# Optimization experiments

Measured on AMD Instinct MI355X. Metric: run time of the kernel, lower is better.

The kernel has to match this reference:

```python
import jax, jax.numpy as jnp
import numpy as np

B = 131072
D = 64
NUM_REL = 32


def setup_inputs() -> dict:
    key = jax.random.key(0)
    k1, k2, k3, k4 = jax.random.split(key, 4)
    embeds1 = jax.random.normal(k1, (B, D), dtype=jnp.float32)
    embeds2 = jax.random.normal(k2, (B, D), dtype=jnp.float32)
    rels = jax.random.randint(k3, (B,), 0, NUM_REL, dtype=jnp.int32)
    # learned relation table: one D*D matrix per relation type
    rel_embeds = jax.random.normal(k4, (NUM_REL, D * D), dtype=jnp.float32)
    return {"embeds1": embeds1, "embeds2": embeds2, "rels": rels,
            "rel_embeds": rel_embeds}


def reference(embeds1, embeds2, rels, rel_embeds):
    # gather per-sample relation matrices: [B, D, D]
    rel_mats = rel_embeds[rels].reshape(-1, D, D)
    # per-sample bilinear form: score_b = e1_b^T R_b e2_b  -> [B]
    e1R = jnp.einsum("bd,bde->be", embeds1, rel_mats)
    return (e1R * embeds2).sum(axis=1)
```

## Files before the change

kernel.cpp:

```cpp
#include <hip/hip_runtime.h>
#include <hip/hip_bf16.h>
#include <cstddef>

#define BB 131072
#define DD 64
#define NREL 32
#define PADN 131584
#define NWAVE (PADN / 16)

#define BLOCKS_AC 512
#define SPB (BB / BLOCKS_AC)
#define CHUNKS 8
#define BPC (BLOCKS_AC / CHUNKS)

typedef __attribute__((ext_vector_type(8))) __bf16 bf16x8;
typedef __attribute__((ext_vector_type(4))) float f32x4;

__global__ __launch_bounds__(256) void phaseR_pre(
    const float* __restrict__ relE, __bf16* __restrict__ Rpre) {
  const int r = blockIdx.x;
  const int t = threadIdx.x;
  const float* __restrict__ R = relE + (size_t)r * (DD * DD);
  __bf16* __restrict__ dst = Rpre + (size_t)r * 8192;
#pragma unroll
  for (int i = 0; i < 16; ++i) {
    const int idx = i * 256 + t;
    const int g = idx >> 9;
    const int lane = (idx >> 3) & 63;
    const int j = idx & 7;
    const int k = (g >> 2) * 32 + (lane >> 4) * 8 + j;
    const int n = (g & 3) * 16 + (lane & 15);
    const float x = R[k * DD + n];
    const __bf16 hb = (__bf16)x;
    dst[idx] = hb;
    dst[4096 + idx] = (__bf16)(x - (float)hb);
  }
}

__global__ __launch_bounds__(256) void phaseA_hist(
    const int* __restrict__ rels, int* __restrict__ blockCnt) {
  __shared__ int hist[NREL];
  const int t = threadIdx.x;
  if (t < NREL) hist[t] = 0;
  __syncthreads();
  atomicAdd(&hist[rels[blockIdx.x * 256 + t]], 1);
  __syncthreads();
  if (t < NREL) blockCnt[blockIdx.x * NREL + t] = hist[t];
}

__global__ __launch_bounds__(256) void phaseB_scan(
    const int* __restrict__ blockCnt, int* __restrict__ blockOff,
    int* __restrict__ binBase, int* __restrict__ permPacked) {
  __shared__ int partial[CHUNKS][NREL];
  __shared__ int chunkBase[CHUNKS][NREL];
  __shared__ int binB[NREL];
  __shared__ int totS[NREL];
  __shared__ int totalPad;
  const int t = threadIdx.x;
  const int c = t >> 5;
  const int r = t & 31;
  const int b0 = c * BPC;
  int run = 0;
#pragma unroll 4
  for (int b = 0; b < BPC; ++b) run += blockCnt[(b0 + b) * NREL + r];
  partial[c][r] = run;
  __syncthreads();
  if (t < NREL) {
    int acc = 0;
#pragma unroll
    for (int i = 0; i < CHUNKS; ++i) { chunkBase[i][t] = acc; acc += partial[i][t]; }
    totS[t] = acc;
  }
  __syncthreads();
  if (t == 0) {
    int acc = 0;
#pragma unroll
    for (int i = 0; i < NREL; ++i) {
      binB[i] = acc;
      acc += (totS[i] + 15) & ~15;
    }
    totalPad = acc;
  }
  __syncthreads();
  if (t < NREL) {
    binBase[t] = binB[t];
    const int start = binB[t] + totS[t];
    const int end = binB[t] + ((totS[t] + 15) & ~15);
    for (int p = start; p < end; ++p) permPacked[p] = -1;
  }
  for (int p = totalPad + t; p < PADN; p += 256) permPacked[p] = -1;
  int run2 = chunkBase[c][r];
#pragma unroll 4
  for (int b = 0; b < BPC; ++b) {
    blockOff[(b0 + b) * NREL + r] = run2;
    run2 += blockCnt[(b0 + b) * NREL + r];
  }
}

__global__ __launch_bounds__(256) void phaseC_scatter(
    const int* __restrict__ rels, const int* __restrict__ blockOff,
    const int* __restrict__ binBase, int* __restrict__ permPacked) {
  __shared__ int cnt[NREL];
  __shared__ int baseArr[NREL];
  const int t = threadIdx.x;
  if (t < NREL) {
    cnt[t] = 0;
    baseArr[t] = binBase[t] + blockOff[blockIdx.x * NREL + t];
  }
  __syncthreads();
  const int s = blockIdx.x * SPB + t;
  const int rv = rels[s];
  const int rank = atomicAdd(&cnt[rv], 1);
  permPacked[baseArr[rv] + rank] = (rv << 17) | s;
}

__global__ __launch_bounds__(64, 4) void bilinear_mfma16(
    const float* __restrict__ e1g, const float* __restrict__ e2g,
    const __bf16* __restrict__ Rpre, const int* __restrict__ permPacked,
    float* __restrict__ out) {
  __shared__ float sA[16 * 65];
  const int lane = threadIdx.x;
  const int l15 = lane & 15;
  const int h2 = lane >> 4;
  const int pk = permPacked[blockIdx.x * 16 + l15];
  const unsigned long long vm = __ballot(pk >= 0);
  if (vm == 0ull) return;
  const int r0 = __builtin_amdgcn_readlane(pk, (int)__builtin_ctzll(vm)) >> 17;

#pragma unroll
  for (int i = 0; i < 16; ++i) {
    const int s = __builtin_amdgcn_readlane(pk, i) & 0x1FFFF;
    sA[i * 65 + lane] = e1g[(size_t)s * DD + lane];
  }
  __syncthreads();

  const bf16x8* __restrict__ bp = (const bf16x8*)(Rpre + (size_t)r0 * 8192);

  f32x4 acc[4];
#pragma unroll
  for (int nt = 0; nt < 4; ++nt)
#pragma unroll
    for (int i = 0; i < 4; ++i) acc[nt][i] = 0.f;

#pragma unroll
  for (int kc = 0; kc < 2; ++kc) {
    bf16x8 aH, aL;
    const float* p = &sA[l15 * 65 + kc * 32 + h2 * 8];
#pragma unroll
    for (int j = 0; j < 8; ++j) {
      const float x = p[j];
      const __bf16 hb = (__bf16)x;
      aH[j] = hb;
      aL[j] = (__bf16)(x - (float)hb);
    }
#pragma unroll
    for (int nt = 0; nt < 4; ++nt) {
      const int g = kc * 4 + nt;
      const bf16x8 bH = bp[g * 64 + lane];
      const bf16x8 bL = bp[512 + g * 64 + lane];
      acc[nt] = __builtin_amdgcn_mfma_f32_16x16x32_bf16(aH, bH, acc[nt], 0, 0, 0);
      acc[nt] = __builtin_amdgcn_mfma_f32_16x16x32_bf16(aH, bL, acc[nt], 0, 0, 0);
      acc[nt] = __builtin_amdgcn_mfma_f32_16x16x32_bf16(aL, bH, acc[nt], 0, 0, 0);
    }
  }

  float rp[4] = {0.f, 0.f, 0.f, 0.f};
#pragma unroll
  for (int reg = 0; reg < 4; ++reg) {
    const int si = __shfl(pk, h2 * 4 + reg) & 0x1FFFF;
    const float* er = e2g + (size_t)si * DD + l15;
#pragma unroll
    for (int nt = 0; nt < 4; ++nt)
      rp[reg] = fmaf(acc[nt][reg], er[nt * 16], rp[reg]);
  }
#pragma unroll
  for (int m = 1; m < 16; m <<= 1)
#pragma unroll
    for (int reg = 0; reg < 4; ++reg) rp[reg] += __shfl_xor(rp[reg], m);
#pragma unroll
  for (int reg = 0; reg < 4; ++reg) {
    const int pkw = __shfl(pk, h2 * 4 + reg);
    if (l15 == reg && pkw >= 0) out[pkw & 0x1FFFF] = rp[reg];
  }
}

extern "C" void kernel_launch(void* const* d_in, const int* in_sizes, int n_in,
                              void* d_out, int out_size, void* d_ws, size_t ws_size,
                              hipStream_t stream) {
  const float* e1 = (const float*)d_in[0];
  const float* e2 = (const float*)d_in[1];
  const int* rels = (const int*)d_in[2];
  const float* relE = (const float*)d_in[3];
  float* out = (float*)d_out;

  int* permPacked = (int*)d_ws;
  int* blockCnt = permPacked + PADN;
  int* blockOff = blockCnt + BLOCKS_AC * NREL;
  int* binBase = blockOff + BLOCKS_AC * NREL;
  __bf16* Rpre = (__bf16*)((char*)d_ws + (1 << 20));

  phaseR_pre<<<NREL, 256, 0, stream>>>(relE, Rpre);
  phaseA_hist<<<BLOCKS_AC, 256, 0, stream>>>(rels, blockCnt);
  phaseB_scan<<<1, 256, 0, stream>>>(blockCnt, blockOff, binBase, permPacked);
  phaseC_scatter<<<BLOCKS_AC, 256, 0, stream>>>(rels, blockOff, binBase, permPacked);
  bilinear_mfma16<<<NWAVE, 64, 0, stream>>>(e1, e2, Rpre, permPacked, out);
}
```

Baseline: 118.3 us.

## Fuse relation preprocessing into histogram kernel and pack four waves per block

The relation-matrix bf16 split is folded into the histogram kernel, which removes one kernel launch. The bilinear kernel now runs four 16-sample waves per 256-thread block and drops the LDS staging of e1 rows. Each lane loads its e1 row directly as float4 vectors and prefetches its e2 values before the MFMA loop. This cuts launch overhead, LDS traffic and the barrier, and lets the e2 loads overlap the matrix work, at the cost of less coalesced direct global loads of e1 and higher register pressure.

```diff
diff --git a/kernel.cpp b/kernel.cpp
--- a/kernel.cpp
+++ b/kernel.cpp
@@ -6,7 +6,7 @@
 #define DD 64
 #define NREL 32
 #define PADN 131584
-#define NWAVE (PADN / 16)
+#define NBLK (PADN / 64)
 
 #define BLOCKS_AC 512
 #define SPB (BB / BLOCKS_AC)
@@ -16,29 +16,9 @@
 typedef __attribute__((ext_vector_type(8))) __bf16 bf16x8;
 typedef __attribute__((ext_vector_type(4))) float f32x4;
 
-__global__ __launch_bounds__(256) void phaseR_pre(
+__global__ __launch_bounds__(256) void phaseA_hist(
+    const int* __restrict__ rels, int* __restrict__ blockCnt,
     const float* __restrict__ relE, __bf16* __restrict__ Rpre) {
-  const int r = blockIdx.x;
-  const int t = threadIdx.x;
-  const float* __restrict__ R = relE + (size_t)r * (DD * DD);
-  __bf16* __restrict__ dst = Rpre + (size_t)r * 8192;
-#pragma unroll
-  for (int i = 0; i < 16; ++i) {
-    const int idx = i * 256 + t;
-    const int g = idx >> 9;
-    const int lane = (idx >> 3) & 63;
-    const int j = idx & 7;
-    const int k = (g >> 2) * 32 + (lane >> 4) * 8 + j;
-    const int n = (g & 3) * 16 + (lane & 15);
-    const float x = R[k * DD + n];
-    const __bf16 hb = (__bf16)x;
-    dst[idx] = hb;
-    dst[4096 + idx] = (__bf16)(x - (float)hb);
-  }
-}
-
-__global__ __launch_bounds__(256) void phaseA_hist(
-    const int* __restrict__ rels, int* __restrict__ blockCnt) {
   __shared__ int hist[NREL];
   const int t = threadIdx.x;
   if (t < NREL) hist[t] = 0;
@@ -46,6 +26,25 @@
   atomicAdd(&hist[rels[blockIdx.x * 256 + t]], 1);
   __syncthreads();
   if (t < NREL) blockCnt[blockIdx.x * NREL + t] = hist[t];
+
+  if (blockIdx.x < NREL) {
+    const int r = blockIdx.x;
+    const float* __restrict__ R = relE + (size_t)r * (DD * DD);
+    __bf16* __restrict__ dst = Rpre + (size_t)r * 8192;
+#pragma unroll
+    for (int i = 0; i < 16; ++i) {
+      const int idx = i * 256 + t;
+      const int g = idx >> 9;
+      const int lane = (idx >> 3) & 63;
+      const int j = idx & 7;
+      const int k = (g >> 2) * 32 + (lane >> 4) * 8 + j;
+      const int n = (g & 3) * 16 + (lane & 15);
+      const float x = R[k * DD + n];
+      const __bf16 hb = (__bf16)x;
+      dst[idx] = hb;
+      dst[4096 + idx] = (__bf16)(x - (float)hb);
+    }
+  }
 }
 
 __global__ __launch_bounds__(256) void phaseB_scan(
@@ -114,25 +113,30 @@
   permPacked[baseArr[rv] + rank] = (rv << 17) | s;
 }
 
-__global__ __launch_bounds__(64, 4) void bilinear_mfma16(
+__global__ __launch_bounds__(256, 4) void bilinear_mfma16(
     const float* __restrict__ e1g, const float* __restrict__ e2g,
     const __bf16* __restrict__ Rpre, const int* __restrict__ permPacked,
     float* __restrict__ out) {
-  __shared__ float sA[16 * 65];
-  const int lane = threadIdx.x;
+  const int lane = threadIdx.x & 63;
+  const int wv = threadIdx.x >> 6;
   const int l15 = lane & 15;
   const int h2 = lane >> 4;
-  const int pk = permPacked[blockIdx.x * 16 + l15];
+  const int pk = permPacked[blockIdx.x * 64 + wv * 16 + l15];
   const unsigned long long vm = __ballot(pk >= 0);
   if (vm == 0ull) return;
   const int r0 = __builtin_amdgcn_readlane(pk, (int)__builtin_ctzll(vm)) >> 17;
 
-#pragma unroll
-  for (int i = 0; i < 16; ++i) {
-    const int s = __builtin_amdgcn_readlane(pk, i) & 0x1FFFF;
-    sA[i * 65 + lane] = e1g[(size_t)s * DD + lane];
-  }
-  __syncthreads();
+  const int sa = __shfl(pk, l15) & 0x1FFFF;
+  const float4* __restrict__ arow = (const float4*)(e1g + (size_t)sa * DD);
+
+  float e2v[4][4];
+#pragma unroll
+  for (int reg = 0; reg < 4; ++reg) {
+    const int si = __shfl(pk, h2 * 4 + reg) & 0x1FFFF;
+    const float* __restrict__ er = e2g + (size_t)si * DD + l15;
+#pragma unroll
+    for (int nt = 0; nt < 4; ++nt) e2v[reg][nt] = er[nt * 16];
+  }
 
   const bf16x8* __restrict__ bp = (const bf16x8*)(Rpre + (size_t)r0 * 8192);
 
@@ -144,14 +148,15 @@
 
 #pragma unroll
   for (int kc = 0; kc < 2; ++kc) {
+    const float4 v0 = arow[kc * 8 + h2 * 2];
+    const float4 v1 = arow[kc * 8 + h2 * 2 + 1];
+    const float x[8] = {v0.x, v0.y, v0.z, v0.w, v1.x, v1.y, v1.z, v1.w};
     bf16x8 aH, aL;
-    const float* p = &sA[l15 * 65 + kc * 32 + h2 * 8];
 #pragma unroll
     for (int j = 0; j < 8; ++j) {
-      const float x = p[j];
-      const __bf16 hb = (__bf16)x;
+      const __bf16 hb = (__bf16)x[j];
       aH[j] = hb;
-      aL[j] = (__bf16)(x - (float)hb);
+      aL[j] = (__bf16)(x[j] - (float)hb);
     }
 #pragma unroll
     for (int nt = 0; nt < 4; ++nt) {
@@ -166,13 +171,10 @@
 
   float rp[4] = {0.f, 0.f, 0.f, 0.f};
 #pragma unroll
-  for (int reg = 0; reg < 4; ++reg) {
-    const int si = __shfl(pk, h2 * 4 + reg) & 0x1FFFF;
-    const float* er = e2g + (size_t)si * DD + l15;
+  for (int reg = 0; reg < 4; ++reg)
 #pragma unroll
     for (int nt = 0; nt < 4; ++nt)
-      rp[reg] = fmaf(acc[nt][reg], er[nt * 16], rp[reg]);
-  }
+      rp[reg] = fmaf(acc[nt][reg], e2v[reg][nt], rp[reg]);
 #pragma unroll
   for (int m = 1; m < 16; m <<= 1)
 #pragma unroll
@@ -199,9 +201,8 @@
   int* binBase = blockOff + BLOCKS_AC * NREL;
   __bf16* Rpre = (__bf16*)((char*)d_ws + (1 << 20));
 
-  phaseR_pre<<<NREL, 256, 0, stream>>>(relE, Rpre);
-  phaseA_hist<<<BLOCKS_AC, 256, 0, stream>>>(rels, blockCnt);
+  phaseA_hist<<<BLOCKS_AC, 256, 0, stream>>>(rels, blockCnt, relE, Rpre);
   phaseB_scan<<<1, 256, 0, stream>>>(blockCnt, blockOff, binBase, permPacked);
   phaseC_scatter<<<BLOCKS_AC, 256, 0, stream>>>(rels, blockOff, binBase, permPacked);
-  bilinear_mfma16<<<NWAVE, 64, 0, stream>>>(e1, e2, Rpre, permPacked, out);
-}
+  bilinear_mfma16<<<NBLK, 256, 0, stream>>>(e1, e2, Rpre, permPacked, out);
+}
```

New measurement: 117.2 us. No clear change (-1.0%).
